# Optimization experiments

Measured on AMD Instinct MI355X. Metric: run time of the kernel, lower is better.

The kernel has to match this reference:

```python
import jax, jax.numpy as jnp
import numpy as np


def lstm(x, W, U, b):
    """Keras LSTM with activation='relu', recurrent_activation='sigmoid'.
    x: [B, S, E]; W: [E, 4u]; U: [u, 4u]; b: [4u]. Gate order i,f,c,o.
    Returns (all hidden states [B,S,u], last hidden [B,u])."""
    B = x.shape[0]
    u = U.shape[0]
    h0 = jnp.zeros((B, u), x.dtype)
    c0 = jnp.zeros((B, u), x.dtype)

    def step(carry, xt):
        h, c = carry
        z = xt @ W + h @ U + b
        i, f, g, o = jnp.split(z, 4, axis=-1)
        i = jax.nn.sigmoid(i)
        f = jax.nn.sigmoid(f)
        g = jax.nn.relu(g)          # candidate activation = relu
        o = jax.nn.sigmoid(o)
        c = f * c + i * g
        h = o * jax.nn.relu(c)      # output activation = relu
        return (h, c), h

    (hT, _), hs = jax.lax.scan(step, (h0, c0), jnp.swapaxes(x, 0, 1))
    return jnp.swapaxes(hs, 0, 1), hT


def setup_inputs() -> dict:
    key = jax.random.key(0)
    ks = iter(jax.random.split(key, 64))

    def W(*s):
        return jax.random.normal(next(ks), s, jnp.float32) * 0.05

    V = 32000
    inp = {
        "t": jax.random.randint(next(ks), (8, 16, 64), 0, V, jnp.int32),
        "p": jax.random.randint(next(ks), (8, 16, 512), 0, V, jnp.int32),
        "emb_t": W(V, 128),
        "emb_p": W(V, 256),
        # title LSTMs: 128 (return_seq) -> 64
        "tl0_W": W(128, 512), "tl0_U": W(128, 512), "tl0_b": jnp.zeros((512,), jnp.float32),
        "tl1_W": W(128, 256), "tl1_U": W(64, 256),  "tl1_b": jnp.zeros((256,), jnp.float32),
        # title dense: 128 relu, 64 relu, 32 linear
        "td0_W": W(64, 128),  "td0_b": jnp.zeros((128,), jnp.float32),
        "td1_W": W(128, 64),  "td1_b": jnp.zeros((64,), jnp.float32),
        "td2_W": W(64, 32),   "td2_b": jnp.zeros((32,), jnp.float32),
        # parag LSTMs: 256 (rs) -> 128 (rs) -> 64
        "pl0_W": W(256, 1024), "pl0_U": W(256, 1024), "pl0_b": jnp.zeros((1024,), jnp.float32),
        "pl1_W": W(256, 512),  "pl1_U": W(128, 512),  "pl1_b": jnp.zeros((512,), jnp.float32),
        "pl2_W": W(128, 256),  "pl2_U": W(64, 256),   "pl2_b": jnp.zeros((256,), jnp.float32),
        # parag dense: 128 relu, 64 relu, 32 linear
        "pd0_W": W(64, 128),  "pd0_b": jnp.zeros((128,), jnp.float32),
        "pd1_W": W(128, 64),  "pd1_b": jnp.zeros((64,), jnp.float32),
        "pd2_W": W(64, 32),   "pd2_b": jnp.zeros((32,), jnp.float32),
        # head: 256 relu, 128 relu, 64 relu, 32 sigmoid
        "L0_W": W(64, 256),  "L0_b": jnp.zeros((256,), jnp.float32),
        "L1_W": W(256, 128), "L1_b": jnp.zeros((128,), jnp.float32),
        "L2_W": W(128, 64),  "L2_b": jnp.zeros((64,), jnp.float32),
        "L3_W": W(64, 32),   "L3_b": jnp.zeros((32,), jnp.float32),
    }
    return inp


def reference(t, p, emb_t, emb_p,
              tl0_W, tl0_U, tl0_b, tl1_W, tl1_U, tl1_b,
              td0_W, td0_b, td1_W, td1_b, td2_W, td2_b,
              pl0_W, pl0_U, pl0_b, pl1_W, pl1_U, pl1_b, pl2_W, pl2_U, pl2_b,
              pd0_W, pd0_b, pd1_W, pd1_b, pd2_W, pd2_b,
              L0_W, L0_b, L1_W, L1_b, L2_W, L2_b, L3_W, L3_b):
    B, N, St = t.shape
    Sp = p.shape[2]

    # The original loops over B and map_fn over a singleton axis; the math is
    # identical to running the stacks on a flattened [B*N] recurrent batch.
    xt = emb_t[t.reshape(B * N, St)]              # [BN, St, 128]
    xt, _ = lstm(xt, tl0_W, tl0_U, tl0_b)         # [BN, St, 128]
    _, ht = lstm(xt, tl1_W, tl1_U, tl1_b)         # [BN, 64]
    ht = jax.nn.relu(ht @ td0_W + td0_b)
    ht = jax.nn.relu(ht @ td1_W + td1_b)
    ht = ht @ td2_W + td2_b                       # [BN, 32] (no activation)

    xp = emb_p[p.reshape(B * N, Sp)]              # [BN, Sp, 256]
    xp, _ = lstm(xp, pl0_W, pl0_U, pl0_b)
    xp, _ = lstm(xp, pl1_W, pl1_U, pl1_b)
    _, hp = lstm(xp, pl2_W, pl2_U, pl2_b)         # [BN, 64]
    hp = jax.nn.relu(hp @ pd0_W + pd0_b)
    hp = jax.nn.relu(hp @ pd1_W + pd1_b)
    hp = hp @ pd2_W + pd2_b                       # [BN, 32]

    feat = jnp.concatenate([ht, hp], axis=-1).reshape(B, N, 64)
    x = feat.mean(axis=1)                         # reduce_mean over axis=-2 (N)
    x = jax.nn.relu(x @ L0_W + L0_b)
    x = jax.nn.relu(x @ L1_W + L1_b)
    x = jax.nn.relu(x @ L2_W + L2_b)
    x = jax.nn.sigmoid(x @ L3_W + L3_b)           # [B, 32]
    return x
```

## Files before the change

### kernel.cpp

```cpp
#include <hip/hip_runtime.h>
#include <hip/hip_fp16.h>

typedef _Float16 f16;
typedef _Float16 f16x8 __attribute__((ext_vector_type(8)));
typedef float    f32x4 __attribute__((ext_vector_type(4)));
typedef unsigned short ushort;
typedef unsigned int uint;
typedef unsigned long long u64;

__device__ __forceinline__ float sigm(float x) { return 1.f / (1.f + __expf(-x)); }
__device__ __forceinline__ float reluf(float x) { return x > 0.f ? x : 0.f; }
__device__ __forceinline__ float h2f(ushort u) { return (float)__builtin_bit_cast(f16, u); }
__device__ __forceinline__ ushort f2h(float v) { return __builtin_bit_cast(ushort, (f16)v); }

#define LDRLX(p)    __hip_atomic_load((p), __ATOMIC_RELAXED, __HIP_MEMORY_SCOPE_AGENT)
#define STRLX(p, v) __hip_atomic_store((p), (v), __ATOMIC_RELAXED, __HIP_MEMORY_SCOPE_AGENT)
#define MFMA16(a, b, c) __builtin_amdgcn_mfma_f32_16x16x32_f16((a), (b), (c), 0, 0, 0)
#define LBAR() do { asm volatile("s_waitcnt lgkmcnt(0)" ::: "memory"); \
                    __builtin_amdgcn_s_barrier(); } while (0)

__device__ __forceinline__ void poll_all(uint* p, uint need, bool act) {
  bool done = !act;
  while (true) {
    if (!done) done = (LDRLX(p) >= need);
    if (__all((int)done)) break;
    __builtin_amdgcn_s_sleep(1);
  }
}

__device__ __forceinline__ u64 ldr64(const u64* p) {
  return __hip_atomic_load(p, __ATOMIC_RELAXED, __HIP_MEMORY_SCOPE_AGENT);
}
__device__ __forceinline__ void str64(u64* p, u64 v) {
  __hip_atomic_store(p, v, __ATOMIC_RELAXED, __HIP_MEMORY_SCOPE_AGENT);
}

template <int NR>
__device__ __forceinline__ void poll_recs(const u64* const (&ra)[NR],
                                          const uint (&nd)[NR], u64 (&rv)[NR]) {
  bool ok[NR];
#pragma unroll
  for (int i = 0; i < NR; i++) ok[i] = (nd[i] == 0u);
  while (true) {
    bool all = true;
#pragma unroll
    for (int i = 0; i < NR; i++) if (!ok[i]) rv[i] = ldr64(ra[i]);
#pragma unroll
    for (int i = 0; i < NR; i++) if (!ok[i]) ok[i] = ((uint)(rv[i] >> 32) >= nd[i]);
#pragma unroll
    for (int i = 0; i < NR; i++) all &= ok[i];
    if (all) return;
    __builtin_amdgcn_s_sleep(1);
  }
}

template <int KF>
__global__ void pack_bsw(const float* __restrict__ B, f16* __restrict__ dst, int N) {
  int id = blockIdx.x * 256 + threadIdx.x;
  int total = KF * 32 * N;
  if (id >= total) return;
  int j  = id & 7;
  int L  = (id >> 3) & 63;
  int r  = id >> 9;
  int kf = r & (KF - 1);
  int c  = r / KF;
  int k  = kf * 32 + ((L >> 4) * 8) + j;
  int n  = c * 16 + (L & 15);
  dst[id] = (f16)B[k * N + n];
}

struct RP {
  const int *t_tok, *p_tok;
  const float *emb_t, *emb_p;
  const f16 *Bp, *Bt;
  const float *tl0_b, *pl0_b;
  f16 *xp2, *xt2;
  const f16 *U0f, *W1f, *U1f, *W2f, *U2f, *U0tf, *W1tf, *U1tf;
  const float *pl1_b, *pl2_b, *tl1_b;
  const float *pd0W, *pd0b, *pd1W, *pd1b, *pd2W, *pd2b;
  const float *td0W, *td0b, *td1W, *td1b, *td2W, *td2b;
  u64 *h0r, *h1r, *h0tr;
  uint *cnt, *xfl, *tfl;
  float* feat;
};

template <int Sx, int K, int KF, int N, int NC, int MODE>
__device__ __forceinline__ void gemm_tile(int g, int t0,
    const int* __restrict__ tok, const float* __restrict__ emb,
    const f16* __restrict__ Bsw, const float* __restrict__ bias,
    u64* __restrict__ X, char* smem) {
  int* tokLds = (int*)smem;
  f16x8* bLds = (f16x8*)(smem + 1024);
  const int tid = threadIdx.x;
  if (tid < 64) {
    int wv = tid >> 4, rho = tid & 15;
    tokLds[tid] = tok[(g * 16 + rho) * Sx + t0 + wv];
  }
  __syncthreads();
  const int wave = tid >> 6, lane = tid & 63;
  const int quad = lane >> 4, l16 = lane & 15;
  f16x8 a[KF];
  {
    const float* arow = emb + (long)tokLds[wave * 16 + l16] * K + quad * 8;
#pragma unroll
    for (int kf = 0; kf < KF; kf++) {
      float4 v0 = *(const float4*)(arow + kf * 32);
      float4 v1 = *(const float4*)(arow + kf * 32 + 4);
      f16x8 tv;
      tv[0] = (f16)v0.x; tv[1] = (f16)v0.y; tv[2] = (f16)v0.z; tv[3] = (f16)v0.w;
      tv[4] = (f16)v1.x; tv[5] = (f16)v1.y; tv[6] = (f16)v1.z; tv[7] = (f16)v1.w;
      a[kf] = tv;
    }
  }
  const int t = t0 + wave;
  const f16x8* Bfrag = (const f16x8*)Bsw;
  for (int c = 0; c < NC; c++) {
    __syncthreads();
    for (int i = tid; i < KF * 64; i += 256) bLds[i] = Bfrag[c * KF * 64 + i];
    __syncthreads();
    f32x4 acc = {0.f, 0.f, 0.f, 0.f};
#pragma unroll
    for (int kf = 0; kf < KF; kf++)
      acc = MFMA16(a[kf], bLds[kf * 64 + lane], acc);
    const int col = c * 16 + l16;
    const float bc = bias[col];
    uint lo = (uint)f2h(acc[0] + bc) | ((uint)f2h(acc[1] + bc) << 16);
    uint hi = (uint)f2h(acc[2] + bc) | ((uint)f2h(acc[3] + bc) << 16);
    u64 pv = (u64)lo | ((u64)hi << 32);
    size_t b64;
    if (MODE == 0) {
      int gm = col >> 8, u = col & 255;
      b64 = (((size_t)(g * 512 + t) * 4 + gm) * 1024) + u * 4 + quad;
    } else {
      int gm = col >> 7, u = col & 127;
      b64 = (((size_t)(g * 64 + t) * 4 + gm) * 512) + u * 4 + quad;
    }
    str64(X + b64, pv);
  }
  __syncthreads();
}

__device__ void worker_body(const RP& A, int wid, char* smem) {
  const int tid = threadIdx.x;
  for (int tile = wid; tile < 1152; tile += 160) {
    if (tile < 128) {
      int tch = tile >> 3, g = tile & 7;
      gemm_tile<64, 128, 4, 512, 32, 1>(g, tch * 4, A.t_tok, A.emb_t, A.Bt,
                                        A.tl0_b, (u64*)A.xt2, smem);
      if (tid == 0) STRLX(A.tfl + g * 16 + tch, 1u);
    } else {
      int m0 = tile - 128, tch = m0 >> 3, g = m0 & 7;
      gemm_tile<512, 256, 8, 1024, 64, 0>(g, tch * 4, A.p_tok, A.emb_p, A.Bp,
                                          A.pl0_b, (u64*)A.xp2, smem);
      if (tid == 0) STRLX(A.xfl + g * 128 + tch, 1u);
    }
  }
}

__global__ __launch_bounds__(256, 1) void fused(RP A) {
  __shared__ __align__(16) char smem[147968];
  const int blk = blockIdx.x;
  if (blk >= 96) { worker_body(A, blk - 96, smem); return; }
  const int tid = threadIdx.x;
  const int w = tid >> 6, lane = tid & 63;
  const int quad = lane >> 4, l16 = lane & 15;
  const int role = blk >> 3, g = blk & 7;
  uint* mytag = A.cnt + (role * 8 + g) * 16;

  if (role < 4) {
    const int bb = role;
    f16* wlds = (f16*)smem;
    f16* hb   = (f16*)(smem + 131072);
    {
      const uint4* U0q = (const uint4*)A.U0f;
      uint4* wq = (uint4*)wlds;
      for (int idx = tid; idx < 8192; idx += 256) {
        int gm = idx >> 11, r = idx & 2047, wv = r >> 9, kf = (r >> 6) & 7, ln = r & 63;
        wq[idx] = U0q[((gm * 16 + 4 * bb + wv) * 8 + kf) * 64 + ln];
      }
    }
    for (int idx = tid; idx < 4224; idx += 256) hb[idx] = (f16)0.f;
    float c0[4] = {0.f, 0.f, 0.f, 0.f};
    u64* ringg = A.h0r + (size_t)g * 16384;
    int pp3[3]; { int q = 0; for (int p = 0; p < 4; p++) if (p != bb) pp3[q++] = p; }
    const u64* xq2 = (const u64*)A.xp2;
    const f16x8* wv8 = (const f16x8*)wlds;
    const int myu = 64 * bb + 16 * w + l16;
    const int ulq = 16 * ((tid >> 4) & 3) + (tid & 15);
    const int qd  = tid >> 6;
    uint* bpp = A.cnt;
    if (lane < 4) bpp = A.cnt + ((4 + lane) * 8 + g) * 16;
    uint* xflg = A.xfl + g * 128;
    __syncthreads();

    for (int t = 0; t < 512; t++) {
      {
        uint* pp = bpp; uint need = 0; bool act = false;
        if (lane < 4) { act = (t > 0) && ((t & 3) == 0); need = t > 4 ? (uint)(t - 4) : 0u; }
        else if (lane == 4) { act = ((t & 3) == 0); need = 1u; pp = xflg + (t >> 2); }
        poll_all(pp, need, act);
      }
      u64 xs[4];
      {
        size_t xb = ((size_t)(g * 512 + t) * 4) * 1024 + (size_t)myu * 4 + quad;
#pragma unroll
        for (int gm = 0; gm < 4; gm++) xs[gm] = ldr64(xq2 + xb + (size_t)gm * 1024);
      }
      {
        const u64* slotb = ringg + (size_t)((t + 7) & 7) * 2048;
        const u64* ra[6]; uint nd[6]; u64 rv[6];
#pragma unroll
        for (int q = 0; q < 3; q++) {
          const u64* rb = slotb + pp3[q] * 512 + 2 * tid;
          ra[q * 2] = rb; ra[q * 2 + 1] = rb + 1;
          nd[q * 2] = nd[q * 2 + 1] = (t > 0) ? (uint)t : 0u;
        }
        poll_recs<6>(ra, nd, rv);
        if (t > 0) {
          f16* dst = hb + (t & 1) * 4224;
#pragma unroll
          for (int q = 0; q < 3; q++)
#pragma unroll
            for (int j = 0; j < 2; j++) {
              uint pay = (uint)rv[q * 2 + j];
              int r0 = qd * 4 + 2 * j;
              dst[r0 * 264 + pp3[q] * 64 + ulq]       = __builtin_bit_cast(f16, (ushort)pay);
              dst[(r0 + 1) * 264 + pp3[q] * 64 + ulq] = __builtin_bit_cast(f16, (ushort)(pay >> 16));
            }
        }
      }
      LBAR();
      f16x8 af[8];
#pragma unroll
      for (int kf = 0; kf < 8; kf++)
        af[kf] = *(const f16x8*)&hb[(t & 1) * 4224 + l16 * 264 + kf * 32 + quad * 8];
      f32x4 z[4];
#pragma unroll
      for (int gm = 0; gm < 4; gm++) {
        f32x4 zz = {0.f, 0.f, 0.f, 0.f};
#pragma unroll
        for (int kf = 0; kf < 8; kf++)
          zz = MFMA16(af[kf], wv8[((gm * 4 + w) * 8 + kf) * 64 + lane], zz);
        z[gm] = zz;
      }
      ushort hs[4];
      f16* wbuf = hb + ((t + 1) & 1) * 4224;
#pragma unroll
      for (int r = 0; r < 4; r++) {
        float gi = sigm(z[0][r] + h2f((ushort)(xs[0] >> (16 * r))));
        float ff = sigm(z[1][r] + h2f((ushort)(xs[1] >> (16 * r))));
        float gg = reluf(z[2][r] + h2f((ushort)(xs[2] >> (16 * r))));
        float oo = sigm(z[3][r] + h2f((ushort)(xs[3] >> (16 * r))));
        c0[r] = ff * c0[r] + gi * gg;
        hs[r] = f2h(oo * reluf(c0[r]));
        wbuf[(quad * 4 + r) * 264 + myu] = __builtin_bit_cast(f16, hs[r]);
      }
      {
        u64 tg = ((u64)(uint)(t + 1)) << 32;
        u64* wb = ringg + (size_t)(t & 7) * 2048 + bb * 512 +
                  quad * 128 + w * 32 + l16 * 2;
        str64(wb,     tg | (u64)((uint)hs[0] | ((uint)hs[1] << 16)));
        str64(wb + 1, tg | (u64)((uint)hs[2] | ((uint)hs[3] << 16)));
      }
    }
  } else if (role < 8) {
    const int bn = role - 4;
    f16* wlds = (f16*)smem;
    f16* h0c  = (f16*)(smem + 98304);
    f16* h1b  = (f16*)(smem + 106752);
    float* zL = (float*)(smem + 115456);
    {
      const uint4* W1q = (const uint4*)A.W1f;
      const uint4* U1q = (const uint4*)A.U1f;
      uint4* wq = (uint4*)wlds;
      for (int idx = tid; idx < 4096; idx += 256) {
        int gm = idx >> 10, r = idx & 1023, j2 = r >> 9, kf = (r >> 6) & 7, ln = r & 63;
        wq[idx] = W1q[((gm * 8 + bn * 2 + j2) * 8 + kf) * 64 + ln];
      }
      for (int idx = tid; idx < 2048; idx += 256) {
        int gm = idx >> 9, r = idx & 511, j2 = r >> 8, kf = (r >> 6) & 3, ln = r & 63;
        wq[4096 + idx] = U1q[((gm * 8 + bn * 2 + j2) * 4 + kf) * 64 + ln];
      }
    }
    for (int idx = tid; idx < 2176; idx += 256) h1b[idx] = (f16)0.f;
    float c1[2] = {0.f, 0.f};
    float bth[4];
    { int un = tid & 31; for (int gm = 0; gm < 4; gm++) bth[gm] = A.pl1_b[gm * 128 + 32 * bn + un]; }
    u64* h0rg = A.h0r + (size_t)g * 16384;
    u64* h1rg = A.h1r + (size_t)g * 8192;
    int pp3[3]; { int q = 0; for (int p = 0; p < 4; p++) if (p != bn) pp3[q++] = p; }
    const f16x8* wv8 = (const f16x8*)wlds;
    uint* bpp = A.cnt + (8 * 8 + g) * 16;
    __syncthreads();

    for (int t = 0; t < 512; t++) {
      {
        bool act = (lane == 0) && ((t & 3) == 0);
        uint need = t > 4 ? (uint)(t - 4) : 0u;
        poll_all(bpp, need, act);
      }
      const u64* ra[11]; uint nd[11]; u64 rv[11];
      {
        const u64* s0b = h0rg + (size_t)(t & 7) * 2048;
#pragma unroll
        for (int e = 0; e < 8; e++) { ra[e] = s0b + tid + 256 * e; nd[e] = (uint)(t + 1); }
        const u64* s1b = h1rg + (size_t)((t + 7) & 7) * 1024;
#pragma unroll
        for (int q = 0; q < 3; q++) { ra[8 + q] = s1b + pp3[q] * 256 + tid; nd[8 + q] = (t > 0) ? (uint)t : 0u; }
      }
      poll_recs<11>(ra, nd, rv);
      {
#pragma unroll
        for (int e = 0; e < 8; e++) {
          int idx = tid + 256 * e;
          int bbq = idx >> 9, r = idx & 511;
          int jj = r & 1, l16c = (r >> 1) & 15, wc = (r >> 5) & 3, qdc = (r >> 7) & 3;
          int col = bbq * 64 + 16 * wc + l16c;
          int r0 = qdc * 4 + 2 * jj;
          uint pay = (uint)rv[e];
          h0c[r0 * 264 + col]       = __builtin_bit_cast(f16, (ushort)pay);
          h0c[(r0 + 1) * 264 + col] = __builtin_bit_cast(f16, (ushort)(pay >> 16));
        }
        if (t > 0) {
          f16* dst = h1b + (t & 1) * 2176;
          int sqc = tid >> 5, unc = tid & 31;
#pragma unroll
          for (int q = 0; q < 3; q++) {
            uint pay = (uint)rv[8 + q];
            dst[sqc * 136 + pp3[q] * 32 + unc]       = __builtin_bit_cast(f16, (ushort)pay);
            dst[(sqc + 8) * 136 + pp3[q] * 32 + unc] = __builtin_bit_cast(f16, (ushort)(pay >> 16));
          }
        }
      }
      LBAR();
      if (tid == 0) STRLX(mytag, (uint)(t + 1));
      f16x8 af0[8], af1[4];
#pragma unroll
      for (int kf = 0; kf < 8; kf++)
        af0[kf] = *(const f16x8*)&h0c[l16 * 264 + kf * 32 + quad * 8];
#pragma unroll
      for (int kf = 0; kf < 4; kf++)
        af1[kf] = *(const f16x8*)&h1b[(t & 1) * 2176 + l16 * 136 + kf * 32 + quad * 8];
#pragma unroll
      for (int j2 = 0; j2 < 2; j2++) {
        f32x4 zz = {0.f, 0.f, 0.f, 0.f};
#pragma unroll
        for (int kf = 0; kf < 8; kf++)
          zz = MFMA16(af0[kf], wv8[((w * 2 + j2) * 8 + kf) * 64 + lane], zz);
#pragma unroll
        for (int kf = 0; kf < 4; kf++)
          zz = MFMA16(af1[kf], wv8[4096 + ((w * 2 + j2) * 4 + kf) * 64 + lane], zz);
#pragma unroll
        for (int r = 0; r < 4; r++)
          zL[(quad * 4 + r) * 132 + w * 32 + j2 * 16 + l16] = zz[r];
      }
      LBAR();
      {
        int sq = tid >> 5, un = tid & 31;
        f16* dst = h1b + ((t + 1) & 1) * 2176;
        ushort hh[2];
#pragma unroll
        for (int e = 0; e < 2; e++) {
          int s = sq + 8 * e;
          float gi = sigm(zL[s * 132 + un] + bth[0]);
          float ff = sigm(zL[s * 132 + 32 + un] + bth[1]);
          float gg = reluf(zL[s * 132 + 64 + un] + bth[2]);
          float oo = sigm(zL[s * 132 + 96 + un] + bth[3]);
          c1[e] = ff * c1[e] + gi * gg;
          float hv = oo * reluf(c1[e]);
          hh[e] = f2h(hv);
          dst[s * 136 + 32 * bn + un] = __builtin_bit_cast(f16, hh[e]);
        }
        u64 tg = ((u64)(uint)(t + 1)) << 32;
        str64(h1rg + (size_t)(t & 7) * 1024 + bn * 256 + tid,
              tg | (u64)((uint)hh[0] | ((uint)hh[1] << 16)));
      }
      LBAR();
    }
  } else if (role == 8) {
    f16* wlds = (f16*)smem;
    f16* h1c  = (f16*)(smem + 98304);
    f16* h2db = (f16*)(smem + 107008);
    {
      const uint4* W2q = (const uint4*)A.W2f;
      const uint4* U2q = (const uint4*)A.U2f;
      uint4* wq = (uint4*)wlds;
      for (int idx = tid; idx < 4096; idx += 256) wq[idx] = W2q[idx];
      for (int idx = tid; idx < 2048; idx += 256) wq[4096 + idx] = U2q[idx];
    }
    for (int idx = tid; idx < 1152; idx += 256) h2db[idx] = (f16)0.f;
    float c2[4] = {0.f, 0.f, 0.f, 0.f};
    float b2[4];
#pragma unroll
    for (int gm = 0; gm < 4; gm++) b2[gm] = A.pl2_b[gm * 64 + 16 * w + l16];
    u64* h1rg = A.h1r + (size_t)g * 8192;
    const f16x8* wv8 = (const f16x8*)wlds;
    __syncthreads();

    for (int t = 0; t < 512; t++) {
      const u64* ra[4]; uint nd[4]; u64 rv[4];
      {
        const u64* s1b = h1rg + (size_t)(t & 7) * 1024;
#pragma unroll
        for (int e = 0; e < 4; e++) { ra[e] = s1b + tid + 256 * e; nd[e] = (uint)(t + 1); }
      }
      poll_recs<4>(ra, nd, rv);
      {
        f16* dst = h1c + (t & 1) * 2176;
#pragma unroll
        for (int e = 0; e < 4; e++) {
          int idx = tid + 256 * e;
          int bq = idx >> 8, r = idx & 255;
          int sqc = r >> 5, unc = r & 31;
          uint pay = (uint)rv[e];
          dst[sqc * 136 + bq * 32 + unc]       = __builtin_bit_cast(f16, (ushort)pay);
          dst[(sqc + 8) * 136 + bq * 32 + unc] = __builtin_bit_cast(f16, (ushort)(pay >> 16));
        }
      }
      LBAR();
      if (tid == 0) STRLX(mytag, (uint)(t + 1));
      f16x8 af0[4], af1[2];
#pragma unroll
      for (int kf = 0; kf < 4; kf++)
        af0[kf] = *(const f16x8*)&h1c[(t & 1) * 2176 + l16 * 136 + kf * 32 + quad * 8];
#pragma unroll
      for (int kf = 0; kf < 2; kf++)
        af1[kf] = *(const f16x8*)&h2db[(t & 1) * 1152 + l16 * 72 + kf * 32 + quad * 8];
      f32x4 z[4];
#pragma unroll
      for (int gm = 0; gm < 4; gm++) {
        f32x4 zz = {0.f, 0.f, 0.f, 0.f};
#pragma unroll
        for (int kf = 0; kf < 4; kf++)
          zz = MFMA16(af0[kf], wv8[((gm * 4 + w) * 4 + kf) * 64 + lane], zz);
#pragma unroll
        for (int kf = 0; kf < 2; kf++)
          zz = MFMA16(af1[kf], wv8[4096 + ((gm * 4 + w) * 2 + kf) * 64 + lane], zz);
        z[gm] = zz;
      }
#pragma unroll
      for (int r = 0; r < 4; r++) {
        float gi = sigm(z[0][r] + b2[0]);
        float ff = sigm(z[1][r] + b2[1]);
        float gg = reluf(z[2][r] + b2[2]);
        float oo = sigm(z[3][r] + b2[3]);
        c2[r] = ff * c2[r] + gi * gg;
        h2db[((t + 1) & 1) * 1152 + (quad * 4 + r) * 72 + 16 * w + l16] = (f16)(oo * reluf(c2[r]));
      }
    }
    __syncthreads();
    float* zmA = (float*)smem;
    float* zmB = (float*)(smem + 8448);
    const f16* hf = h2db;
#pragma unroll 1
    for (int e = 0; e < 8; e++) {
      const int idx = tid + 256 * e, sq = idx >> 7, j = idx & 127;
      float a = A.pd0b[j];
      for (int k = 0; k < 64; k++) a += (float)hf[sq * 72 + k] * A.pd0W[k * 128 + j];
      zmA[sq * 132 + j] = reluf(a);
    }
    __syncthreads();
#pragma unroll 1
    for (int e = 0; e < 4; e++) {
      const int idx = tid + 256 * e, sq = idx >> 6, j = idx & 63;
      float a = A.pd1b[j];
      for (int k = 0; k < 128; k++) a += zmA[sq * 132 + k] * A.pd1W[k * 64 + j];
      zmB[sq * 68 + j] = reluf(a);
    }
    __syncthreads();
#pragma unroll 1
    for (int e = 0; e < 2; e++) {
      const int idx = tid + 256 * e, sq = idx >> 5, j = idx & 31;
      float a = A.pd2b[j];
      for (int k = 0; k < 64; k++) a += zmB[sq * 68 + k] * A.pd2W[k * 32 + j];
      A.feat[(g * 16 + sq) * 64 + 32 + j] = a;
    }
  } else if (role < 11) {
    const int bb = role - 9;
    f16* wlds = (f16*)smem;
    f16* hb   = (f16*)(smem + 65536);
    {
      const uint4* U0tq = (const uint4*)A.U0tf;
      uint4* wq = (uint4*)wlds;
      for (int idx = tid; idx < 4096; idx += 256) {
        int gm = idx >> 10, r = idx & 1023, wv = r >> 8, kf = (r >> 6) & 3, ln = r & 63;
        wq[idx] = U0tq[((gm * 8 + 4 * bb + wv) * 4 + kf) * 64 + ln];
      }
    }
    for (int idx = tid; idx < 2176; idx += 256) hb[idx] = (f16)0.f;
    float c0[4] = {0.f, 0.f, 0.f, 0.f};
    u64* ringg = A.h0tr + (size_t)g * 8192;
    const u64* xtq = (const u64*)A.xt2;
    const f16x8* wv8 = (const f16x8*)wlds;
    const int myu = 64 * bb + 16 * w + l16;
    const int pbb = bb ^ 1;
    uint* bpp = A.cnt + (11 * 8 + g) * 16;
    uint* tflg = A.tfl + g * 16;
    __syncthreads();

    for (int t = 0; t < 64; t++) {
      {
        uint* pp = bpp; uint need = 0; bool act = false;
        if (lane == 0) { act = (t > 0) && ((t & 3) == 0); need = t > 4 ? (uint)(t - 4) : 0u; }
        else if (lane == 1) { act = ((t & 3) == 0); need = 1u; pp = tflg + (t >> 2); }
        poll_all(pp, need, act);
      }
      u64 xs[4];
      {
        size_t xb = ((size_t)(g * 64 + t) * 4) * 512 + (size_t)myu * 4 + quad;
#pragma unroll
        for (int gm = 0; gm < 4; gm++) xs[gm] = ldr64(xtq + xb + (size_t)gm * 512);
      }
      {
        const u64* ra[2]; uint nd[2]; u64 rv[2];
        const u64* rb = ringg + (size_t)((t + 7) & 7) * 1024 + pbb * 512 + 2 * tid;
        ra[0] = rb; ra[1] = rb + 1;
        nd[0] = nd[1] = (t > 0) ? (uint)t : 0u;
        poll_recs<2>(ra, nd, rv);
        if (t > 0) {
          f16* dst = hb + (t & 1) * 2176;
          const int ul = tid >> 2;
#pragma unroll
          for (int j = 0; j < 2; j++) {
            uint pay = (uint)rv[j];
            int r0 = ((tid & 3) * 2 + j) * 2;
            dst[r0 * 136 + pbb * 64 + ul]       = __builtin_bit_cast(f16, (ushort)pay);
            dst[(r0 + 1) * 136 + pbb * 64 + ul] = __builtin_bit_cast(f16, (ushort)(pay >> 16));
          }
        }
      }
      LBAR();
      f16x8 af[4];
#pragma unroll
      for (int kf = 0; kf < 4; kf++)
        af[kf] = *(const f16x8*)&hb[(t & 1) * 2176 + l16 * 136 + kf * 32 + quad * 8];
      f32x4 z[4];
#pragma unroll
      for (int gm = 0; gm < 4; gm++) {
        f32x4 zz = {0.f, 0.f, 0.f, 0.f};
#pragma unroll
        for (int kf = 0; kf < 4; kf++)
          zz = MFMA16(af[kf], wv8[((gm * 4 + w) * 4 + kf) * 64 + lane], zz);
        z[gm] = zz;
      }
      ushort hs[4];
      f16* wbuf = hb + ((t + 1) & 1) * 2176;
#pragma unroll
      for (int r = 0; r < 4; r++) {
        float gi = sigm(z[0][r] + h2f((ushort)(xs[0] >> (16 * r))));
        float ff = sigm(z[1][r] + h2f((ushort)(xs[1] >> (16 * r))));
        float gg = reluf(z[2][r] + h2f((ushort)(xs[2] >> (16 * r))));
        float oo = sigm(z[3][r] + h2f((ushort)(xs[3] >> (16 * r))));
        c0[r] = ff * c0[r] + gi * gg;
        hs[r] = f2h(oo * reluf(c0[r]));
        wbuf[(quad * 4 + r) * 136 + myu] = __builtin_bit_cast(f16, hs[r]);
      }
      {
        u64 tg = ((u64)(uint)(t + 1)) << 32;
        u64* wb = ringg + (size_t)(t & 7) * 1024 + bb * 512 + (16 * w + l16) * 8 + quad * 2;
        str64(wb,     tg | (u64)((uint)hs[0] | ((uint)hs[1] << 16)));
        str64(wb + 1, tg | (u64)((uint)hs[2] | ((uint)hs[3] << 16)));
      }
    }
  } else {
    f16* wlds = (f16*)smem;
    f16* h0tc = (f16*)(smem + 98304);
    f16* h1db = (f16*)(smem + 107008);
    {
      const uint4* W1tq = (const uint4*)A.W1tf;
      const uint4* U1tq = (const uint4*)A.U1tf;
      uint4* wq = (uint4*)wlds;
      for (int idx = tid; idx < 4096; idx += 256) wq[idx] = W1tq[idx];
      for (int idx = tid; idx < 2048; idx += 256) wq[4096 + idx] = U1tq[idx];
    }
    for (int idx = tid; idx < 1152; idx += 256) h1db[idx] = (f16)0.f;
    float c1[4] = {0.f, 0.f, 0.f, 0.f};
    float bt[4];
#pragma unroll
    for (int gm = 0; gm < 4; gm++) bt[gm] = A.tl1_b[gm * 64 + 16 * w + l16];
    u64* ringg = A.h0tr + (size_t)g * 8192;
    const f16x8* wv8 = (const f16x8*)wlds;
    __syncthreads();

    for (int t = 0; t < 64; t++) {
      const u64* ra[4]; uint nd[4]; u64 rv[4];
      {
        const u64* base = ringg + (size_t)(t & 7) * 1024;
#pragma unroll
        for (int e = 0; e < 4; e++) { ra[e] = base + tid + 256 * e; nd[e] = (uint)(t + 1); }
      }
      poll_recs<4>(ra, nd, rv);
      {
        f16* dst = h0tc + (t & 1) * 2176;
#pragma unroll
        for (int e = 0; e < 4; e++) {
          int idx = tid + 256 * e;
          int q = idx >> 9, rr = idx & 511, uls = rr >> 3, rp = rr & 7;
          uint pay = (uint)rv[e];
          dst[(2 * rp) * 136 + q * 64 + uls]     = __builtin_bit_cast(f16, (ushort)pay);
          dst[(2 * rp + 1) * 136 + q * 64 + uls] = __builtin_bit_cast(f16, (ushort)(pay >> 16));
        }
      }
      LBAR();
      if (tid == 0) STRLX(mytag, (uint)(t + 1));
      f16x8 af0[4], af1[2];
#pragma unroll
      for (int kf = 0; kf < 4; kf++)
        af0[kf] = *(const f16x8*)&h0tc[(t & 1) * 2176 + l16 * 136 + kf * 32 + quad * 8];
#pragma unroll
      for (int kf = 0; kf < 2; kf++)
        af1[kf] = *(const f16x8*)&h1db[(t & 1) * 1152 + l16 * 72 + kf * 32 + quad * 8];
      f32x4 z[4];
#pragma unroll
      for (int gm = 0; gm < 4; gm++) {
        f32x4 zz = {0.f, 0.f, 0.f, 0.f};
#pragma unroll
        for (int kf = 0; kf < 4; kf++)
          zz = MFMA16(af0[kf], wv8[((gm * 4 + w) * 4 + kf) * 64 + lane], zz);
#pragma unroll
        for (int kf = 0; kf < 2; kf++)
          zz = MFMA16(af1[kf], wv8[4096 + ((gm * 4 + w) * 2 + kf) * 64 + lane], zz);
        z[gm] = zz;
      }
#pragma unroll
      for (int r = 0; r < 4; r++) {
        float gi = sigm(z[0][r] + bt[0]);
        float ff = sigm(z[1][r] + bt[1]);
        float gg = reluf(z[2][r] + bt[2]);
        float oo = sigm(z[3][r] + bt[3]);
        c1[r] = ff * c1[r] + gi * gg;
        h1db[((t + 1) & 1) * 1152 + (quad * 4 + r) * 72 + 16 * w + l16] = (f16)(oo * reluf(c1[r]));
      }
    }
    __syncthreads();
    float* zmA = (float*)smem;
    float* zmB = (float*)(smem + 8448);
    const f16* hf = h1db;
#pragma unroll 1
    for (int e = 0; e < 8; e++) {
      const int idx = tid + 256 * e, sq = idx >> 7, j = idx & 127;
      float a = A.td0b[j];
      for (int k = 0; k < 64; k++) a += (float)hf[sq * 72 + k] * A.td0W[k * 128 + j];
      zmA[sq * 132 + j] = reluf(a);
    }
    __syncthreads();
#pragma unroll 1
    for (int e = 0; e < 4; e++) {
      const int idx = tid + 256 * e, sq = idx >> 6, j = idx & 63;
      float a = A.td1b[j];
      for (int k = 0; k < 128; k++) a += zmA[sq * 132 + k] * A.td1W[k * 64 + j];
      zmB[sq * 68 + j] = reluf(a);
    }
    __syncthreads();
#pragma unroll 1
    for (int e = 0; e < 2; e++) {
      const int idx = tid + 256 * e, sq = idx >> 5, j = idx & 31;
      float a = A.td2b[j];
      for (int k = 0; k < 64; k++) a += zmB[sq * 68 + k] * A.td2W[k * 32 + j];
      A.feat[(g * 16 + sq) * 64 + j] = a;
    }
  }
}

__global__ __launch_bounds__(256) void head_kernel(const float* __restrict__ feat,
    const float* __restrict__ L0W, const float* __restrict__ L0b,
    const float* __restrict__ L1W, const float* __restrict__ L1b,
    const float* __restrict__ L2W, const float* __restrict__ L2b,
    const float* __restrict__ L3W, const float* __restrict__ L3b,
    float* __restrict__ out) {
  __shared__ float xb[512];
  __shared__ float y0[2048];
  __shared__ float y1[1024];
  __shared__ float y2[512];
  const int tid = threadIdx.x;
  for (int idx = tid; idx < 512; idx += 256) {
    int b = idx >> 6, d = idx & 63;
    float s = 0.f;
    for (int n = 0; n < 16; n++) s += feat[(b * 16 + n) * 64 + d];
    xb[idx] = s * (1.f / 16.f);
  }
  __syncthreads();
  for (int idx = tid; idx < 2048; idx += 256) {
    int b = idx >> 8, j = idx & 255;
    float a = L0b[j];
    for (int k = 0; k < 64; k++) a += xb[b * 64 + k] * L0W[k * 256 + j];
    y0[idx] = reluf(a);
  }
  __syncthreads();
  for (int idx = tid; idx < 1024; idx += 256) {
    int b = idx >> 7, j = idx & 127;
    float a = L1b[j];
    for (int k = 0; k < 256; k++) a += y0[b * 256 + k] * L1W[k * 128 + j];
    y1[idx] = reluf(a);
  }
  __syncthreads();
  for (int idx = tid; idx < 512; idx += 256) {
    int b = idx >> 6, j = idx & 63;
    float a = L2b[j];
    for (int k = 0; k < 128; k++) a += y1[b * 128 + k] * L2W[k * 64 + j];
    y2[idx] = reluf(a);
  }
  __syncthreads();
  {
    int b = tid >> 5, j = tid & 31;
    float a = L3b[j];
    for (int k = 0; k < 64; k++) a += y2[b * 64 + k] * L3W[k * 32 + j];
    out[b * 32 + j] = 1.f / (1.f + __expf(-a));
  }
}

extern "C" void kernel_launch(void* const* d_in, const int* in_sizes, int n_in,
                              void* d_out, int out_size, void* d_ws, size_t ws_size,
                              hipStream_t stream) {
  const int*   t_tok = (const int*)d_in[0];
  const int*   p_tok = (const int*)d_in[1];
  const float* emb_t = (const float*)d_in[2];
  const float* emb_p = (const float*)d_in[3];
  const float* tl0_W = (const float*)d_in[4];
  const float* tl0_U = (const float*)d_in[5];
  const float* tl0_b = (const float*)d_in[6];
  const float* tl1_W = (const float*)d_in[7];
  const float* tl1_U = (const float*)d_in[8];
  const float* tl1_b = (const float*)d_in[9];
  const float* td0_W = (const float*)d_in[10];
  const float* td0_b = (const float*)d_in[11];
  const float* td1_W = (const float*)d_in[12];
  const float* td1_b = (const float*)d_in[13];
  const float* td2_W = (const float*)d_in[14];
  const float* td2_b = (const float*)d_in[15];
  const float* pl0_W = (const float*)d_in[16];
  const float* pl0_U = (const float*)d_in[17];
  const float* pl0_b = (const float*)d_in[18];
  const float* pl1_W = (const float*)d_in[19];
  const float* pl1_U = (const float*)d_in[20];
  const float* pl1_b = (const float*)d_in[21];
  const float* pl2_W = (const float*)d_in[22];
  const float* pl2_U = (const float*)d_in[23];
  const float* pl2_b = (const float*)d_in[24];
  const float* pd0_W = (const float*)d_in[25];
  const float* pd0_b = (const float*)d_in[26];
  const float* pd1_W = (const float*)d_in[27];
  const float* pd1_b = (const float*)d_in[28];
  const float* pd2_W = (const float*)d_in[29];
  const float* pd2_b = (const float*)d_in[30];
  const float* L0_W  = (const float*)d_in[31];
  const float* L0_b  = (const float*)d_in[32];
  const float* L1_W  = (const float*)d_in[33];
  const float* L1_b  = (const float*)d_in[34];
  const float* L2_W  = (const float*)d_in[35];
  const float* L2_b  = (const float*)d_in[36];
  const float* L3_W  = (const float*)d_in[37];
  const float* L3_b  = (const float*)d_in[38];

  char* ws = (char*)d_ws;
  size_t off = 0;
  auto alloc = [&](size_t bytes) {
    void* ptr = ws + off;
    off += (bytes + 255) & ~(size_t)255;
    return ptr;
  };
  f16* xp2  = (f16*)alloc((size_t)8 * 512 * 4 * 4096 * 2);
  f16* xt2  = (f16*)alloc((size_t)8 * 64 * 4 * 2048 * 2);
  f16* Bp   = (f16*)alloc((size_t)256 * 1024 * 2);
  f16* Bt   = (f16*)alloc((size_t)128 * 512 * 2);
  f16* U0f  = (f16*)alloc((size_t)256 * 1024 * 2);
  f16* W1f  = (f16*)alloc((size_t)256 * 512 * 2);
  f16* U1f  = (f16*)alloc((size_t)128 * 512 * 2);
  f16* W2f  = (f16*)alloc((size_t)128 * 256 * 2);
  f16* U2f  = (f16*)alloc((size_t)64 * 256 * 2);
  f16* U0tf = (f16*)alloc((size_t)128 * 512 * 2);
  f16* W1tf = (f16*)alloc((size_t)128 * 256 * 2);
  f16* U1tf = (f16*)alloc((size_t)64 * 256 * 2);
  size_t ringoff = off;
  u64* h0r  = (u64*)alloc((size_t)8 * 16384 * 8);
  u64* h1r  = (u64*)alloc((size_t)8 * 8192 * 8);
  u64* h0tr = (u64*)alloc((size_t)8 * 8192 * 8);
  uint* cnt = (uint*)alloc((size_t)96 * 16 * 4);
  uint* xfl = (uint*)alloc((size_t)8 * 128 * 4);
  uint* tfl = (uint*)alloc((size_t)8 * 16 * 4);
  size_t ringlen = off - ringoff;
  float* feat = (float*)alloc((size_t)128 * 64 * 4);

  hipMemsetAsync(ws + ringoff, 0, ringlen, stream);

  pack_bsw<4><<<256, 256, 0, stream>>>(tl0_W, Bt, 512);
  pack_bsw<8><<<1024, 256, 0, stream>>>(pl0_W, Bp, 1024);
  pack_bsw<8><<<1024, 256, 0, stream>>>(pl0_U, U0f, 1024);
  pack_bsw<8><<<512, 256, 0, stream>>>(pl1_W, W1f, 512);
  pack_bsw<4><<<256, 256, 0, stream>>>(pl1_U, U1f, 512);
  pack_bsw<4><<<128, 256, 0, stream>>>(pl2_W, W2f, 256);
  pack_bsw<2><<<64, 256, 0, stream>>>(pl2_U, U2f, 256);
  pack_bsw<4><<<256, 256, 0, stream>>>(tl0_U, U0tf, 512);
  pack_bsw<4><<<128, 256, 0, stream>>>(tl1_W, W1tf, 256);
  pack_bsw<2><<<64, 256, 0, stream>>>(tl1_U, U1tf, 256);

  RP ra;
  ra.t_tok = t_tok; ra.p_tok = p_tok; ra.emb_t = emb_t; ra.emb_p = emb_p;
  ra.Bp = Bp; ra.Bt = Bt; ra.tl0_b = tl0_b; ra.pl0_b = pl0_b;
  ra.xp2 = xp2; ra.xt2 = xt2;
  ra.U0f = U0f; ra.W1f = W1f; ra.U1f = U1f; ra.W2f = W2f; ra.U2f = U2f;
  ra.U0tf = U0tf; ra.W1tf = W1tf; ra.U1tf = U1tf;
  ra.pl1_b = pl1_b; ra.pl2_b = pl2_b; ra.tl1_b = tl1_b;
  ra.pd0W = pd0_W; ra.pd0b = pd0_b; ra.pd1W = pd1_W; ra.pd1b = pd1_b;
  ra.pd2W = pd2_W; ra.pd2b = pd2_b;
  ra.td0W = td0_W; ra.td0b = td0_b; ra.td1W = td1_W; ra.td1b = td1_b;
  ra.td2W = td2_W; ra.td2b = td2_b;
  ra.h0r = h0r; ra.h1r = h1r; ra.h0tr = h0tr;
  ra.cnt = cnt; ra.xfl = xfl; ra.tfl = tfl;
  ra.feat = feat;
  fused<<<256, 256, 0, stream>>>(ra);

  head_kernel<<<1, 256, 0, stream>>>(feat, L0_W, L0_b, L1_W, L1_b, L2_W, L2_b,
                                     L3_W, L3_b, (float*)d_out);
}
```

Baseline: 1.409 ms.

## Merge pack/memset launches into one prep kernel and fuse head into persistent kernel

```diff
diff --git a/kernel.cpp b/kernel.cpp
--- a/kernel.cpp
+++ b/kernel.cpp
@@ -19,6 +19,13 @@
 #define LBAR() do { asm volatile("s_waitcnt lgkmcnt(0)" ::: "memory"); \
                     __builtin_amdgcn_s_barrier(); } while (0)
 
+__device__ __forceinline__ float ldf(const float* p) {
+  return __hip_atomic_load(p, __ATOMIC_RELAXED, __HIP_MEMORY_SCOPE_AGENT);
+}
+__device__ __forceinline__ void stf(float* p, float v) {
+  __hip_atomic_store(p, v, __ATOMIC_RELAXED, __HIP_MEMORY_SCOPE_AGENT);
+}
+
 __device__ __forceinline__ void poll_all(uint* p, uint need, bool act) {
   bool done = !act;
   while (true) {
@@ -54,19 +61,40 @@
   }
 }
 
-template <int KF>
-__global__ void pack_bsw(const float* __restrict__ B, f16* __restrict__ dst, int N) {
-  int id = blockIdx.x * 256 + threadIdx.x;
-  int total = KF * 32 * N;
-  if (id >= total) return;
-  int j  = id & 7;
-  int L  = (id >> 3) & 63;
-  int r  = id >> 9;
-  int kf = r & (KF - 1);
-  int c  = r / KF;
-  int k  = kf * 32 + ((L >> 4) * 8) + j;
-  int n  = c * 16 + (L & 15);
-  dst[id] = (f16)B[k * N + n];
+struct PrepA {
+  const float* src[10];
+  f16* dst[10];
+  int kfm[10];
+  int lg[10];
+  int nn[10];
+  int total[10];
+  int bo[10];
+  int packBlocks;
+  u64* zb;
+  long zn;
+};
+
+__global__ __launch_bounds__(256) void prep(PrepA P) {
+  const int blk = blockIdx.x;
+  if (blk < P.packBlocks) {
+    int r = 0;
+#pragma unroll
+    for (int i = 1; i < 10; i++) if (blk >= P.bo[i]) r = i;
+    int id = (blk - P.bo[r]) * 256 + threadIdx.x;
+    if (id < P.total[r]) {
+      int j  = id & 7;
+      int L  = (id >> 3) & 63;
+      int rr = id >> 9;
+      int kf = rr & P.kfm[r];
+      int c  = rr >> P.lg[r];
+      int k  = kf * 32 + ((L >> 4) * 8) + j;
+      int n  = c * 16 + (L & 15);
+      P.dst[r][id] = (f16)P.src[r][k * P.nn[r] + n];
+    }
+  } else {
+    long i = (long)(blk - P.packBlocks) * 256 + threadIdx.x;
+    if (i < P.zn) P.zb[i] = 0;
+  }
 }
 
 struct RP {
@@ -79,9 +107,11 @@
   const float *pl1_b, *pl2_b, *tl1_b;
   const float *pd0W, *pd0b, *pd1W, *pd1b, *pd2W, *pd2b;
   const float *td0W, *td0b, *td1W, *td1b, *td2W, *td2b;
+  const float *L0W, *L0b, *L1W, *L1b, *L2W, *L2b, *L3W, *L3b;
   u64 *h0r, *h1r, *h0tr;
-  uint *cnt, *xfl, *tfl;
+  uint *cnt, *xfl, *tfl, *ffl;
   float* feat;
+  float* out;
 };
 
 template <int Sx, int K, int KF, int N, int NC, int MODE>
@@ -140,6 +170,51 @@
   __syncthreads();
 }
 
+__device__ void head_body(const RP& A, char* smem) {
+  const int tid = threadIdx.x;
+  const int lane = tid & 63;
+  poll_all(A.ffl + (lane & 15), 1u, lane < 16);
+  __syncthreads();
+  float* xb = (float*)smem;
+  float* y0 = (float*)(smem + 2048);
+  float* y1 = (float*)(smem + 10240);
+  float* y2 = (float*)(smem + 14336);
+  for (int idx = tid; idx < 512; idx += 256) {
+    int b = idx >> 6, d = idx & 63;
+    float s = 0.f;
+    for (int n = 0; n < 16; n++) s += ldf(A.feat + (b * 16 + n) * 64 + d);
+    xb[idx] = s * (1.f / 16.f);
+  }
+  __syncthreads();
+  for (int idx = tid; idx < 2048; idx += 256) {
+    int b = idx >> 8, j = idx & 255;
+    float a = A.L0b[j];
+    for (int k = 0; k < 64; k++) a += xb[b * 64 + k] * A.L0W[k * 256 + j];
+    y0[idx] = reluf(a);
+  }
+  __syncthreads();
+  for (int idx = tid; idx < 1024; idx += 256) {
+    int b = idx >> 7, j = idx & 127;
+    float a = A.L1b[j];
+    for (int k = 0; k < 256; k++) a += y0[b * 256 + k] * A.L1W[k * 128 + j];
+    y1[idx] = reluf(a);
+  }
+  __syncthreads();
+  for (int idx = tid; idx < 512; idx += 256) {
+    int b = idx >> 6, j = idx & 63;
+    float a = A.L2b[j];
+    for (int k = 0; k < 128; k++) a += y1[b * 128 + k] * A.L2W[k * 64 + j];
+    y2[idx] = reluf(a);
+  }
+  __syncthreads();
+  {
+    int b = tid >> 5, j = tid & 31;
+    float a = A.L3b[j];
+    for (int k = 0; k < 64; k++) a += y2[b * 64 + k] * A.L3W[k * 32 + j];
+    A.out[b * 32 + j] = 1.f / (1.f + __expf(-a));
+  }
+}
+
 __device__ void worker_body(const RP& A, int wid, char* smem) {
   const int tid = threadIdx.x;
   for (int tile = wid; tile < 1152; tile += 160) {
@@ -155,6 +230,7 @@
       if (tid == 0) STRLX(A.xfl + g * 128 + tch, 1u);
     }
   }
+  if (wid == 159) head_body(A, smem);
 }
 
 __global__ __launch_bounds__(256, 1) void fused(RP A) {
@@ -473,8 +549,10 @@
       const int idx = tid + 256 * e, sq = idx >> 5, j = idx & 31;
       float a = A.pd2b[j];
       for (int k = 0; k < 64; k++) a += zmB[sq * 68 + k] * A.pd2W[k * 32 + j];
-      A.feat[(g * 16 + sq) * 64 + 32 + j] = a;
-    }
+      stf(A.feat + (g * 16 + sq) * 64 + 32 + j, a);
+    }
+    __syncthreads();
+    if (tid == 0) STRLX(A.ffl + 8 + g, 1u);
   } else if (role < 11) {
     const int bb = role - 9;
     f16* wlds = (f16*)smem;
@@ -657,55 +735,10 @@
       const int idx = tid + 256 * e, sq = idx >> 5, j = idx & 31;
       float a = A.td2b[j];
       for (int k = 0; k < 64; k++) a += zmB[sq * 68 + k] * A.td2W[k * 32 + j];
-      A.feat[(g * 16 + sq) * 64 + j] = a;
-    }
-  }
-}
-
-__global__ __launch_bounds__(256) void head_kernel(const float* __restrict__ feat,
-    const float* __restrict__ L0W, const float* __restrict__ L0b,
-    const float* __restrict__ L1W, const float* __restrict__ L1b,
-    const float* __restrict__ L2W, const float* __restrict__ L2b,
-    const float* __restrict__ L3W, const float* __restrict__ L3b,
-    float* __restrict__ out) {
-  __shared__ float xb[512];
-  __shared__ float y0[2048];
-  __shared__ float y1[1024];
-  __shared__ float y2[512];
-  const int tid = threadIdx.x;
-  for (int idx = tid; idx < 512; idx += 256) {
-    int b = idx >> 6, d = idx & 63;
-    float s = 0.f;
-    for (int n = 0; n < 16; n++) s += feat[(b * 16 + n) * 64 + d];
-    xb[idx] = s * (1.f / 16.f);
-  }
-  __syncthreads();
-  for (int idx = tid; idx < 2048; idx += 256) {
-    int b = idx >> 8, j = idx & 255;
-    float a = L0b[j];
-    for (int k = 0; k < 64; k++) a += xb[b * 64 + k] * L0W[k * 256 + j];
-    y0[idx] = reluf(a);
-  }
-  __syncthreads();
-  for (int idx = tid; idx < 1024; idx += 256) {
-    int b = idx >> 7, j = idx & 127;
-    float a = L1b[j];
-    for (int k = 0; k < 256; k++) a += y0[b * 256 + k] * L1W[k * 128 + j];
-    y1[idx] = reluf(a);
-  }
-  __syncthreads();
-  for (int idx = tid; idx < 512; idx += 256) {
-    int b = idx >> 6, j = idx & 63;
-    float a = L2b[j];
-    for (int k = 0; k < 128; k++) a += y1[b * 128 + k] * L2W[k * 64 + j];
-    y2[idx] = reluf(a);
-  }
-  __syncthreads();
-  {
-    int b = tid >> 5, j = tid & 31;
-    float a = L3b[j];
-    for (int k = 0; k < 64; k++) a += y2[b * 64 + k] * L3W[k * 32 + j];
-    out[b * 32 + j] = 1.f / (1.f + __expf(-a));
+      stf(A.feat + (g * 16 + sq) * 64 + j, a);
+    }
+    __syncthreads();
+    if (tid == 0) STRLX(A.ffl + g, 1u);
   }
 }
 
@@ -778,21 +811,31 @@
   uint* cnt = (uint*)alloc((size_t)96 * 16 * 4);
   uint* xfl = (uint*)alloc((size_t)8 * 128 * 4);
   uint* tfl = (uint*)alloc((size_t)8 * 16 * 4);
+  uint* ffl = (uint*)alloc((size_t)16 * 4);
   size_t ringlen = off - ringoff;
   float* feat = (float*)alloc((size_t)128 * 64 * 4);
 
-  hipMemsetAsync(ws + ringoff, 0, ringlen, stream);
-
-  pack_bsw<4><<<256, 256, 0, stream>>>(tl0_W, Bt, 512);
-  pack_bsw<8><<<1024, 256, 0, stream>>>(pl0_W, Bp, 1024);
-  pack_bsw<8><<<1024, 256, 0, stream>>>(pl0_U, U0f, 1024);
-  pack_bsw<8><<<512, 256, 0, stream>>>(pl1_W, W1f, 512);
-  pack_bsw<4><<<256, 256, 0, stream>>>(pl1_U, U1f, 512);
-  pack_bsw<4><<<128, 256, 0, stream>>>(pl2_W, W2f, 256);
-  pack_bsw<2><<<64, 256, 0, stream>>>(pl2_U, U2f, 256);
-  pack_bsw<4><<<256, 256, 0, stream>>>(tl0_U, U0tf, 512);
-  pack_bsw<4><<<128, 256, 0, stream>>>(tl1_W, W1tf, 256);
-  pack_bsw<2><<<64, 256, 0, stream>>>(tl1_U, U1tf, 256);
+  PrepA pa;
+  const float* srcs[10] = {tl0_W, pl0_W, pl0_U, pl1_W, pl1_U, pl2_W, pl2_U,
+                           tl0_U, tl1_W, tl1_U};
+  f16* dsts[10] = {Bt, Bp, U0f, W1f, U1f, W2f, U2f, U0tf, W1tf, U1tf};
+  int kfs[10]   = {4, 8, 8, 8, 4, 4, 2, 4, 4, 2};
+  int ns[10]    = {512, 1024, 1024, 512, 512, 256, 256, 512, 256, 256};
+  int bsum = 0;
+  for (int r = 0; r < 10; r++) {
+    pa.src[r] = srcs[r]; pa.dst[r] = dsts[r];
+    pa.kfm[r] = kfs[r] - 1;
+    pa.lg[r]  = (kfs[r] == 8) ? 3 : (kfs[r] == 4 ? 2 : 1);
+    pa.nn[r]  = ns[r];
+    pa.total[r] = kfs[r] * 32 * ns[r];
+    pa.bo[r] = bsum;
+    bsum += pa.total[r] / 256;
+  }
+  pa.packBlocks = bsum;
+  pa.zb = (u64*)(ws + ringoff);
+  pa.zn = (long)(ringlen / 8);
+  int zblocks = (int)((pa.zn + 255) / 256);
+  prep<<<pa.packBlocks + zblocks, 256, 0, stream>>>(pa);
 
   RP ra;
   ra.t_tok = t_tok; ra.p_tok = p_tok; ra.emb_t = emb_t; ra.emb_p = emb_p;
@@ -805,11 +848,11 @@
   ra.pd2W = pd2_W; ra.pd2b = pd2_b;
   ra.td0W = td0_W; ra.td0b = td0_b; ra.td1W = td1_W; ra.td1b = td1_b;
   ra.td2W = td2_W; ra.td2b = td2_b;
+  ra.L0W = L0_W; ra.L0b = L0_b; ra.L1W = L1_W; ra.L1b = L1_b;
+  ra.L2W = L2_W; ra.L2b = L2_b; ra.L3W = L3_W; ra.L3b = L3_b;
   ra.h0r = h0r; ra.h1r = h1r; ra.h0tr = h0tr;
-  ra.cnt = cnt; ra.xfl = xfl; ra.tfl = tfl;
+  ra.cnt = cnt; ra.xfl = xfl; ra.tfl = tfl; ra.ffl = ffl;
   ra.feat = feat;
+  ra.out = (float*)d_out;
   fused<<<256, 256, 0, stream>>>(ra);
-
-  head_kernel<<<1, 256, 0, stream>>>(feat, L0_W, L0_b, L1_W, L1_b, L2_W, L2_b,
-                                     L3_W, L3_b, (float*)d_out);
-}
+}
```

New measurement: 1.387 ms. No clear change (-1.5%).
